# Kernel tuning notes

Measured on AMD Instinct MI355X. Metric: run time of the kernel, lower is better.

The kernel has to match this reference:

```python
import jax, jax.numpy as jnp
import numpy as np

N = 50000
E = 800000
IN = 128
H = 128
OUT = 64
L = 2
THETA = 1.0
SCALE = 2.0


def setup_inputs() -> dict:
    key = jax.random.key(0)
    ks = jax.random.split(key, 12)
    g = lambda k, s: (jax.random.normal(k, s, jnp.float32) * 0.05)
    return {
        "x": jax.random.normal(ks[0], (N, IN), jnp.float32),
        "edge_index": jax.random.randint(ks[1], (2, E), 0, N),
        "mlp_w1": g(ks[2], (IN, 512)), "mlp_b1": jnp.zeros((512,), jnp.float32),
        "mlp_w2": g(ks[3], (512, 64)), "mlp_b2": jnp.zeros((64,), jnp.float32),
        "mlp_w3": g(ks[4], (64, OUT)), "mlp_b3": jnp.zeros((OUT,), jnp.float32),
        "parsing": jnp.ones((L, OUT, OUT), jnp.float32) / SCALE,
        "lin0_w": g(ks[5], (IN, H)), "lin0_b": jnp.zeros((H,), jnp.float32),
        "lin1_w": g(ks[6], (H, OUT)), "lin1_b": jnp.zeros((OUT,), jnp.float32),
        "conv_w1": g(ks[7], (L, H, H)),
        "conv_w2": g(ks[8], (L, H, H)),
    }


def reference(x, edge_index, mlp_w1, mlp_b1, mlp_w2, mlp_b2, mlp_w3, mlp_b3,
              parsing, lin0_w, lin0_b, lin1_w, lin1_b, conv_w1, conv_w2):
    row, col = edge_index[0], edge_index[1]  # start, end

    # --- learn_soft_edge3 (algebraically exact reduction of outer-product + bmm + diag) ---
    h = jax.nn.relu(x @ mlp_w1 + mlp_b1)
    h = jax.nn.relu(h @ mlp_w2 + mlp_b2)
    logits = h @ mlp_w3 + mlp_b3                      # [N, OUT]
    P = jax.nn.relu(SCALE * parsing[0])               # [OUT, OUT]
    # diag(outer(start,end) @ P)[e,c] = start[e,c] * (end @ P)[e,c]
    ew = jnp.sum(logits[row] * (logits @ P)[col], axis=1)  # [E]
    mean = ew.mean()
    var = jnp.var(ew, ddof=1)                          # torch.var is unbiased
    ew = (ew - mean) * jnp.sqrt(jnp.float32(1e-4) / var) + 1.0

    # --- GCN2 stack ---
    x0 = jax.nn.relu(x @ lin0_w + lin0_b)              # [N, H]
    # gcn_norm with self loops (weight 1)
    loop = jnp.arange(N)
    r = jnp.concatenate([row, loop])
    c = jnp.concatenate([col, loop])
    w = jnp.concatenate([ew, jnp.ones((N,), ew.dtype)])
    deg = jax.ops.segment_sum(w, c, num_segments=N)
    dinv = jnp.where(deg > 0, jax.lax.rsqrt(jnp.where(deg > 0, deg, 1.0)), 0.0)
    norm = dinv[r] * w * dinv[c]                       # [E+N]

    hcur = x0
    alpha = 0.0
    for ln in range(L):
        agg = jax.ops.segment_sum(norm[:, None] * hcur[r], c, num_segments=N)  # [N, H]
        agg = agg * (1.0 - alpha)
        x0a = alpha * x0
        beta = float(np.log(THETA / (ln + 1) + 1.0))
        out = (1.0 - beta) * agg + beta * (agg @ conv_w1[ln]) \
            + (1.0 - beta) * x0a + beta * (x0a @ conv_w2[ln])
        hcur = jax.nn.relu(out)
    return hcur @ lin1_w + lin1_b                      # [N, OUT]
```

## Files before the change

### kernel.cpp

```cpp
#include <hip/hip_runtime.h>
#include <hip/hip_bf16.h>
#include <hip/hip_fp16.h>
#include <math.h>

#define NN 50000
#define NE 800000

typedef __attribute__((ext_vector_type(8))) short bf16x8;
typedef __attribute__((ext_vector_type(4))) float f32x4;

__device__ __forceinline__ short f2bf(float f){
  unsigned u = __float_as_uint(f);
  unsigned r = (u + 0x7fffu + ((u >> 16) & 1u)) >> 16;
  return (short)r;
}
__device__ __forceinline__ float bf2f(short s){
  return __uint_as_float(((unsigned)(unsigned short)s) << 16);
}

__device__ __forceinline__ unsigned f2fp8(float f){
  __half h = __float2half(f * 0.00390625f);
  unsigned hb = (unsigned)__half_as_ushort(h);
  unsigned s = hb >> 15;
  unsigned mag = hb & 0x7fffu;
  mag = mag + 0x3fu + ((mag >> 7) & 1u);
  unsigned m8 = mag >> 7;
  if (m8 > 0x7eu) m8 = 0x7eu;
  return (s << 7) | m8;
}
__device__ __forceinline__ void fp8x4_dec(unsigned u, float2& lo, float2& hi){
  unsigned l = ((u & 0x80u) << 8) | ((u & 0x7fu) << 7)
             | ((u & 0x8000u) << 16) | ((u & 0x7f00u) << 15);
  unsigned h = ((u & 0x800000u) >> 8) | ((u & 0x7f0000u) >> 9)
             | (u & 0x80000000u) | ((u & 0x7f000000u) >> 1);
  __half2 hl = *(__half2*)&l;
  __half2 hh = *(__half2*)&h;
  lo = __half22float2(hl);
  hi = __half22float2(hh);
}
__device__ __forceinline__ float fp8_dot4(unsigned a, unsigned b){
  float2 al, ah, bl, bh;
  fp8x4_dec(a, al, ah); fp8x4_dec(b, bl, bh);
  return al.x*bl.x + al.y*bl.y + ah.x*bh.x + ah.y*bh.y;
}

__global__ __launch_bounds__(256) void prep_k(const float* __restrict__ w1,
    const float* __restrict__ w2, const float* __restrict__ w3, const float* __restrict__ pars,
    const float* __restrict__ b3, const float* __restrict__ lin0w, const float* __restrict__ cw1,
    const float* __restrict__ lin1w,
    short* __restrict__ w1t, short* __restrict__ w2t, short* __restrict__ w3t,
    short* __restrict__ w3pt, float* __restrict__ b3P,
    short* __restrict__ lin0wt, short* __restrict__ cw1t0, short* __restrict__ cw1t1,
    short* __restrict__ lin1wt, int* __restrict__ cnt, float* __restrict__ scal){
  int idx = blockIdx.x*256 + threadIdx.x;
  if (idx < NN) cnt[idx] = 0;
  if (idx < 16) scal[idx] = 0.0f;
  if (idx < 65536){
    int n = idx >> 7, k = idx & 127;
    w1t[idx] = f2bf(w1[k*512 + n]);
  } else if (idx < 98304){
    int i = idx - 65536; int n = i >> 9, k = i & 511;
    w2t[i] = f2bf(w2[k*64 + n]);
  } else if (idx < 102400){
    int i = idx - 98304; int n = i >> 6, k = i & 63;
    w3t[i] = f2bf(w3[k*64 + n]);
  } else if (idx < 106496){
    int i = idx - 102400; int c = i >> 6, k = i & 63;
    float s = 0.f;
    for (int j = 0; j < 64; j++)
      s += w3[k*64 + j] * fmaxf(2.f*pars[j*64 + c], 0.f);
    w3pt[i] = f2bf(s);
  } else if (idx < 122880){
    int i = idx - 106496; int n = i >> 7, k = i & 127;
    lin0wt[i] = f2bf(lin0w[k*128 + n]);
  } else if (idx < 139264){
    int i = idx - 122880; int n = i >> 7, k = i & 127;
    cw1t0[i] = f2bf(cw1[k*128 + n]);
  } else if (idx < 155648){
    int i = idx - 139264; int n = i >> 7, k = i & 127;
    cw1t1[i] = f2bf(cw1[16384 + k*128 + n]);
  } else if (idx < 163840){
    int i = idx - 155648; int n = i >> 7, k = i & 127;
    lin1wt[i] = f2bf(lin1w[k*64 + n]);
  } else if (idx < 163904){
    int c = idx - 163840;
    float s = 0.f;
    for (int j = 0; j < 64; j++) s += b3[j] * fmaxf(2.f*pars[j*64 + c], 0.f);
    b3P[c] = s;
  }
}

__global__ __launch_bounds__(256) void mlp_mfma_k(
    const float* __restrict__ x,
    const short* __restrict__ w1t, const float* __restrict__ b1,
    const short* __restrict__ w2t, const float* __restrict__ b2,
    const short* __restrict__ w3t, const float* __restrict__ b3,
    const short* __restrict__ w3pt, const float* __restrict__ b3P,
    unsigned char* __restrict__ lg8, unsigned char* __restrict__ lgp8,
    short* __restrict__ xb, int M)
{
  __shared__ short xs [64][132];
  __shared__ short h1s[64][260];
  __shared__ short h2s[64][68];
  __shared__ short lgs[64][68];
  const int t = threadIdx.x;
  const int wave = t >> 6, lane = t & 63;
  const int quad = lane >> 4, l16 = lane & 15;
  const int m0 = blockIdx.x * 64;

  for (int task = t; task < 1024; task += 256){
    int row = task >> 4, c0 = (task & 15) * 8;
    float4 v0 = make_float4(0,0,0,0), v1 = v0;
    int gm = m0 + row;
    if (gm < M){
      v0 = *(const float4*)(x + (size_t)gm*128 + c0);
      v1 = *(const float4*)(x + (size_t)gm*128 + c0 + 4);
    }
    bf16x8 s;
    s[0]=f2bf(v0.x); s[1]=f2bf(v0.y); s[2]=f2bf(v0.z); s[3]=f2bf(v0.w);
    s[4]=f2bf(v1.x); s[5]=f2bf(v1.y); s[6]=f2bf(v1.z); s[7]=f2bf(v1.w);
    *(bf16x8*)&xs[row][c0] = s;
    if (gm < M) *(bf16x8*)(xb + (size_t)gm*128 + c0) = s;
  }
  __syncthreads();

  f32x4 acc2a[4], acc2b[4];
  #pragma unroll
  for (int mt=0;mt<4;mt++){ acc2a[mt] = (f32x4){0.f,0.f,0.f,0.f}; acc2b[mt] = acc2a[mt]; }
  const int n2 = wave*16 + l16;

  #pragma unroll
  for (int half = 0; half < 2; half++){
    {
      f32x4 acc[4][4];
      #pragma unroll
      for (int mt=0;mt<4;mt++)
        #pragma unroll
        for (int nt=0;nt<4;nt++) acc[mt][nt] = (f32x4){0.f,0.f,0.f,0.f};
      #pragma unroll
      for (int k0 = 0; k0 < 128; k0 += 32){
        bf16x8 a0 = *(const bf16x8*)&xs[l16     ][k0 + quad*8];
        bf16x8 a1 = *(const bf16x8*)&xs[16 + l16][k0 + quad*8];
        bf16x8 a2 = *(const bf16x8*)&xs[32 + l16][k0 + quad*8];
        bf16x8 a3 = *(const bf16x8*)&xs[48 + l16][k0 + quad*8];
        #pragma unroll
        for (int nt = 0; nt < 4; nt++){
          int n = half*256 + wave*64 + nt*16 + l16;
          bf16x8 b = *(const bf16x8*)(w1t + (size_t)n*128 + k0 + quad*8);
          acc[0][nt] = __builtin_amdgcn_mfma_f32_16x16x32_bf16(a0, b, acc[0][nt], 0,0,0);
          acc[1][nt] = __builtin_amdgcn_mfma_f32_16x16x32_bf16(a1, b, acc[1][nt], 0,0,0);
          acc[2][nt] = __builtin_amdgcn_mfma_f32_16x16x32_bf16(a2, b, acc[2][nt], 0,0,0);
          acc[3][nt] = __builtin_amdgcn_mfma_f32_16x16x32_bf16(a3, b, acc[3][nt], 0,0,0);
        }
      }
      #pragma unroll
      for (int nt = 0; nt < 4; nt++){
        int n  = half*256 + wave*64 + nt*16 + l16;
        int cl = wave*64 + nt*16 + l16;
        float bb = b1[n];
        #pragma unroll
        for (int mt = 0; mt < 4; mt++){
          #pragma unroll
          for (int r = 0; r < 4; r++){
            int row = mt*16 + quad*4 + r;
            h1s[row][cl] = f2bf(fmaxf(acc[mt][nt][r] + bb, 0.f));
          }
        }
      }
    }
    __syncthreads();

    #pragma unroll
    for (int k0 = 0; k0 < 128; k0 += 32){
      bf16x8 bA = *(const bf16x8*)(w2t + (size_t)n2*512 + half*256 + k0 + quad*8);
      bf16x8 bB = *(const bf16x8*)(w2t + (size_t)n2*512 + half*256 + 128 + k0 + quad*8);
      #pragma unroll
      for (int mt = 0; mt < 4; mt++){
        bf16x8 aA = *(const bf16x8*)&h1s[mt*16 + l16][k0 + quad*8];
        bf16x8 aB = *(const bf16x8*)&h1s[mt*16 + l16][128 + k0 + quad*8];
        acc2a[mt] = __builtin_amdgcn_mfma_f32_16x16x32_bf16(aA, bA, acc2a[mt], 0,0,0);
        acc2b[mt] = __builtin_amdgcn_mfma_f32_16x16x32_bf16(aB, bB, acc2b[mt], 0,0,0);
      }
    }
    if (half == 0) __syncthreads();
  }

  {
    float bb = b2[n2];
    #pragma unroll
    for (int mt = 0; mt < 4; mt++)
      #pragma unroll
      for (int r = 0; r < 4; r++)
        h2s[mt*16 + quad*4 + r][n2] = f2bf(fmaxf(acc2a[mt][r] + acc2b[mt][r] + bb, 0.f));
  }
  __syncthreads();

  {
    f32x4 accL[4], accP[4];
    #pragma unroll
    for (int mt=0;mt<4;mt++){ accL[mt] = (f32x4){0.f,0.f,0.f,0.f}; accP[mt] = accL[mt]; }
    #pragma unroll
    for (int k0 = 0; k0 < 64; k0 += 32){
      bf16x8 bL = *(const bf16x8*)(w3t  + (size_t)n2*64 + k0 + quad*8);
      bf16x8 bP = *(const bf16x8*)(w3pt + (size_t)n2*64 + k0 + quad*8);
      #pragma unroll
      for (int mt = 0; mt < 4; mt++){
        bf16x8 a = *(const bf16x8*)&h2s[mt*16 + l16][k0 + quad*8];
        accL[mt] = __builtin_amdgcn_mfma_f32_16x16x32_bf16(a, bL, accL[mt], 0,0,0);
        accP[mt] = __builtin_amdgcn_mfma_f32_16x16x32_bf16(a, bP, accP[mt], 0,0,0);
      }
    }
    __syncthreads();
    float bbL = b3[n2], bbP = b3P[n2];
    #pragma unroll
    for (int mt = 0; mt < 4; mt++)
      #pragma unroll
      for (int r = 0; r < 4; r++){
        lgs[mt*16 + quad*4 + r][n2] = f2bf(accL[mt][r] + bbL);
        h2s[mt*16 + quad*4 + r][n2] = f2bf(accP[mt][r] + bbP);
      }
  }
  __syncthreads();

  {
    int row = t >> 2, c0 = (t & 3) * 16;
    int gm = m0 + row;
    if (gm < M){
      const short* pl = &lgs[row][c0];
      const short* pp = &h2s[row][c0];
      unsigned a[4] = {0,0,0,0}, b[4] = {0,0,0,0};
      #pragma unroll
      for (int q2 = 0; q2 < 4; q2++){
        #pragma unroll
        for (int j = 0; j < 4; j++){
          a[q2] |= f2fp8(bf2f(pl[q2*4+j])) << (8*j);
          b[q2] |= f2fp8(bf2f(pp[q2*4+j])) << (8*j);
        }
      }
      uint4 av; av.x=a[0]; av.y=a[1]; av.z=a[2]; av.w=a[3];
      uint4 bv; bv.x=b[0]; bv.y=b[1]; bv.z=b[2]; bv.w=b[3];
      *(uint4*)(lg8  + (size_t)gm*64 + c0) = av;
      *(uint4*)(lgp8 + (size_t)gm*64 + c0) = bv;
    }
  }
}

template<int NT, bool RELU, bool RESID, bool BF16OUT, bool SCALEROW>
__global__ __launch_bounds__(256) void bgemm_k(
    const short* __restrict__ A, const short* __restrict__ Bt,
    const float* __restrict__ bias, const short* __restrict__ extra,
    const float* __restrict__ dinvp,
    float* __restrict__ C, short* __restrict__ Cb, int M, float beta)
{
  const int N = NT*64;
  __shared__ short As[32][132];
  const int t = threadIdx.x;
  const int wave = t >> 6, lane = t & 63;
  const int quad = lane >> 4, l16 = lane & 15;
  const int m0 = blockIdx.x * 32;

  for (int task = t; task < 512; task += 256){
    int row = task >> 4, c0 = (task & 15) * 8;
    bf16x8 v = {0,0,0,0,0,0,0,0};
    if (m0 + row < M) v = *(const bf16x8*)(A + (size_t)(m0+row)*128 + c0);
    *(bf16x8*)&As[row][c0] = v;
  }
  __syncthreads();

  f32x4 acc[2][NT];
  #pragma unroll
  for (int mt=0;mt<2;mt++)
    #pragma unroll
    for (int nt=0;nt<NT;nt++) acc[mt][nt] = (f32x4){0.f,0.f,0.f,0.f};

  #pragma unroll
  for (int k0 = 0; k0 < 128; k0 += 32){
    bf16x8 a0 = *(const bf16x8*)&As[l16     ][k0 + quad*8];
    bf16x8 a1 = *(const bf16x8*)&As[16 + l16][k0 + quad*8];
    #pragma unroll
    for (int nt = 0; nt < NT; nt++){
      int n = (wave*NT + nt)*16 + l16;
      bf16x8 b = *(const bf16x8*)(Bt + (size_t)n*128 + k0 + quad*8);
      acc[0][nt] = __builtin_amdgcn_mfma_f32_16x16x32_bf16(a0, b, acc[0][nt], 0,0,0);
      acc[1][nt] = __builtin_amdgcn_mfma_f32_16x16x32_bf16(a1, b, acc[1][nt], 0,0,0);
    }
  }

  #pragma unroll
  for (int nt = 0; nt < NT; nt++){
    int n = (wave*NT + nt)*16 + l16;
    float bb = (bias != nullptr) ? bias[n] : 0.f;
    #pragma unroll
    for (int mt = 0; mt < 2; mt++){
      #pragma unroll
      for (int r = 0; r < 4; r++){
        int gm = m0 + mt*16 + quad*4 + r;
        if (gm >= M) continue;
        float v = acc[mt][nt][r];
        if (RESID){
          float ex = bf2f(extra[(size_t)gm*N + n]);
          v = beta*v + (1.f - beta)*ex;
        }
        v += bb;
        if (RELU) v = fmaxf(v, 0.f);
        if (SCALEROW) v *= dinvp[gm];
        if (BF16OUT) Cb[(size_t)gm*N + n] = f2bf(v);
        else         C [(size_t)gm*N + n] = v;
      }
    }
  }
}

__global__ __launch_bounds__(256) void bgemm_fuse_k(
    const short* __restrict__ A, const short* __restrict__ Bt,
    const short* __restrict__ extra,
    const short* __restrict__ lin1wt, const float* __restrict__ lin1b,
    float* __restrict__ out, int M, float beta)
{
  __shared__ short As[32][132];
  const int t = threadIdx.x;
  const int wave = t >> 6, lane = t & 63;
  const int quad = lane >> 4, l16 = lane & 15;
  const int m0 = blockIdx.x * 32;

  for (int task = t; task < 512; task += 256){
    int row = task >> 4, c0 = (task & 15) * 8;
    bf16x8 v = {0,0,0,0,0,0,0,0};
    if (m0 + row < M) v = *(const bf16x8*)(A + (size_t)(m0+row)*128 + c0);
    *(bf16x8*)&As[row][c0] = v;
  }
  __syncthreads();

  f32x4 acc[2][2];
  #pragma unroll
  for (int mt=0;mt<2;mt++)
    #pragma unroll
    for (int nt=0;nt<2;nt++) acc[mt][nt] = (f32x4){0.f,0.f,0.f,0.f};

  #pragma unroll
  for (int k0 = 0; k0 < 128; k0 += 32){
    bf16x8 a0 = *(const bf16x8*)&As[l16     ][k0 + quad*8];
    bf16x8 a1 = *(const bf16x8*)&As[16 + l16][k0 + quad*8];
    #pragma unroll
    for (int nt = 0; nt < 2; nt++){
      int n = (wave*2 + nt)*16 + l16;
      bf16x8 b = *(const bf16x8*)(Bt + (size_t)n*128 + k0 + quad*8);
      acc[0][nt] = __builtin_amdgcn_mfma_f32_16x16x32_bf16(a0, b, acc[0][nt], 0,0,0);
      acc[1][nt] = __builtin_amdgcn_mfma_f32_16x16x32_bf16(a1, b, acc[1][nt], 0,0,0);
    }
  }
  __syncthreads();

  #pragma unroll
  for (int nt = 0; nt < 2; nt++){
    int n = (wave*2 + nt)*16 + l16;
    #pragma unroll
    for (int mt = 0; mt < 2; mt++){
      #pragma unroll
      for (int r = 0; r < 4; r++){
        int row = mt*16 + quad*4 + r;
        int gm = m0 + row;
        float v = 0.f;
        if (gm < M){
          float ex = bf2f(extra[(size_t)gm*128 + n]);
          v = fmaxf(beta*acc[mt][nt][r] + (1.f - beta)*ex, 0.f);
        }
        As[row][n] = f2bf(v);
      }
    }
  }
  __syncthreads();

  f32x4 acc2[2];
  acc2[0] = (f32x4){0.f,0.f,0.f,0.f}; acc2[1] = acc2[0];
  const int n2 = wave*16 + l16;
  #pragma unroll
  for (int k0 = 0; k0 < 128; k0 += 32){
    bf16x8 b  = *(const bf16x8*)(lin1wt + (size_t)n2*128 + k0 + quad*8);
    bf16x8 a0 = *(const bf16x8*)&As[l16     ][k0 + quad*8];
    bf16x8 a1 = *(const bf16x8*)&As[16 + l16][k0 + quad*8];
    acc2[0] = __builtin_amdgcn_mfma_f32_16x16x32_bf16(a0, b, acc2[0], 0,0,0);
    acc2[1] = __builtin_amdgcn_mfma_f32_16x16x32_bf16(a1, b, acc2[1], 0,0,0);
  }
  float bb = lin1b[n2];
  #pragma unroll
  for (int mt = 0; mt < 2; mt++)
    #pragma unroll
    for (int r = 0; r < 4; r++){
      int gm = m0 + mt*16 + quad*4 + r;
      if (gm < M) out[(size_t)gm*64 + n2] = acc2[mt][r] + bb;
    }
}

__global__ __launch_bounds__(256) void count_k(const int* __restrict__ col, int* __restrict__ cnt,
    int* __restrict__ rank, int E){
  int i = (blockIdx.x*256 + threadIdx.x)*4;
  if (i + 3 < E){
    int4 c = *(const int4*)(col + i);
    int r0 = atomicAdd(&cnt[c.x], 1);
    int r1 = atomicAdd(&cnt[c.y], 1);
    int r2 = atomicAdd(&cnt[c.z], 1);
    int r3 = atomicAdd(&cnt[c.w], 1);
    *(int4*)(rank + i) = make_int4(r0, r1, r2, r3);
  } else {
    for (; i < E; i++) rank[i] = atomicAdd(&cnt[col[i]], 1);
  }
}

__global__ __launch_bounds__(256) void scan_sums_k(const int* __restrict__ cnt, int* __restrict__ bsum, int n){
  __shared__ int s[256];
  const int t = threadIdx.x;
  int i = blockIdx.x*1024 + t*4;
  int4 v = make_int4(0,0,0,0);
  if (i + 3 < n) v = *(const int4*)(cnt + i);
  else {
    if (i   < n) v.x = cnt[i];
    if (i+1 < n) v.y = cnt[i+1];
    if (i+2 < n) v.z = cnt[i+2];
    if (i+3 < n) v.w = cnt[i+3];
  }
  s[t] = v.x + v.y + v.z + v.w;
  __syncthreads();
  for (int st = 128; st; st >>= 1){
    if (t < st) s[t] += s[t + st];
    __syncthreads();
  }
  if (t == 0) bsum[blockIdx.x] = s[0];
}

__global__ __launch_bounds__(256) void scan_final_k(const int* __restrict__ cnt, const int* __restrict__ bsum,
    int* __restrict__ off, int n, int total, int nb){
  __shared__ int s[256];
  __shared__ int basebs;
  const int t = threadIdx.x;
  if (t < 64){
    int v = (t < nb && t < (int)blockIdx.x) ? bsum[t] : 0;
    #pragma unroll
    for (int o = 1; o < 64; o <<= 1) v += __shfl_xor(v, o);
    if (t == 0) basebs = v;
  }
  int i = blockIdx.x*1024 + t*4;
  int4 v = make_int4(0,0,0,0);
  if (i + 3 < n) v = *(const int4*)(cnt + i);
  else {
    if (i   < n) v.x = cnt[i];
    if (i+1 < n) v.y = cnt[i+1];
    if (i+2 < n) v.z = cnt[i+2];
    if (i+3 < n) v.w = cnt[i+3];
  }
  int tsum = v.x + v.y + v.z + v.w;
  s[t] = tsum;
  __syncthreads();
  #pragma unroll
  for (int st = 1; st < 256; st <<= 1){
    int a = (t >= st) ? s[t - st] : 0;
    __syncthreads();
    s[t] += a;
    __syncthreads();
  }
  int base = s[t] - tsum + basebs;
  int o0 = base, o1 = o0 + v.x, o2 = o1 + v.y, o3 = o2 + v.z;
  if (i   < n) off[i]   = o0;
  if (i+1 < n) off[i+1] = o1;
  if (i+2 < n) off[i+2] = o2;
  if (i+3 < n) off[i+3] = o3;
  if (blockIdx.x == 0 && t == 0) off[n] = total;
}

__global__ __launch_bounds__(256) void scatter_k(const int* __restrict__ row, const int* __restrict__ col,
    const int* __restrict__ off, const int* __restrict__ rank,
    int2* __restrict__ csr_sd, int E){
  int i = (blockIdx.x*256 + threadIdx.x)*4;
  if (i + 3 < E){
    int4 r = *(const int4*)(row + i);
    int4 c = *(const int4*)(col + i);
    int4 k = *(const int4*)(rank + i);
    int o0 = off[c.x], o1 = off[c.y], o2 = off[c.z], o3 = off[c.w];
    int2 p0; p0.x = r.x; p0.y = c.x;
    int2 p1; p1.x = r.y; p1.y = c.y;
    int2 p2; p2.x = r.z; p2.y = c.z;
    int2 p3; p3.x = r.w; p3.y = c.w;
    csr_sd[o0 + k.x] = p0;
    csr_sd[o1 + k.y] = p1;
    csr_sd[o2 + k.z] = p2;
    csr_sd[o3 + k.w] = p3;
  } else {
    for (; i < E; i++){
      int2 p; p.x = row[i]; p.y = col[i];
      csr_sd[off[col[i]] + rank[i]] = p;
    }
  }
}

__global__ __launch_bounds__(256) void ew2_k(const unsigned char* __restrict__ lg8,
    const unsigned char* __restrict__ lgp8,
    const int2* __restrict__ sd,
    float* __restrict__ w, float* __restrict__ scal, int E){
  const int t = threadIdx.x;
  const int lane = t & 63, wid = t >> 6;
  const int g = lane >> 4, q = lane & 15;
  const int gid = (blockIdx.x*4 + wid)*4 + g;
  const int ngroups = gridDim.x*16;
  float s = 0.f, ss = 0.f;
  for (int base = gid*8; base < E; base += ngroups*8){
    int4 p01 = *(const int4*)(sd + base);
    int4 p23 = *(const int4*)(sd + base + 2);
    int4 p45 = *(const int4*)(sd + base + 4);
    int4 p67 = *(const int4*)(sd + base + 6);
    unsigned a0 = *(const unsigned*)(lg8  + (size_t)p01.x*64 + q*4);
    unsigned a1 = *(const unsigned*)(lg8  + (size_t)p01.z*64 + q*4);
    unsigned a2 = *(const unsigned*)(lg8  + (size_t)p23.x*64 + q*4);
    unsigned a3 = *(const unsigned*)(lg8  + (size_t)p23.z*64 + q*4);
    unsigned a4 = *(const unsigned*)(lg8  + (size_t)p45.x*64 + q*4);
    unsigned a5 = *(const unsigned*)(lg8  + (size_t)p45.z*64 + q*4);
    unsigned a6 = *(const unsigned*)(lg8  + (size_t)p67.x*64 + q*4);
    unsigned a7 = *(const unsigned*)(lg8  + (size_t)p67.z*64 + q*4);
    unsigned b0 = *(const unsigned*)(lgp8 + (size_t)p01.y*64 + q*4);
    unsigned b1 = *(const unsigned*)(lgp8 + (size_t)p01.w*64 + q*4);
    unsigned b2 = *(const unsigned*)(lgp8 + (size_t)p23.y*64 + q*4);
    unsigned b3 = *(const unsigned*)(lgp8 + (size_t)p23.w*64 + q*4);
    unsigned b4 = *(const unsigned*)(lgp8 + (size_t)p45.y*64 + q*4);
    unsigned b5 = *(const unsigned*)(lgp8 + (size_t)p45.w*64 + q*4);
    unsigned b6 = *(const unsigned*)(lgp8 + (size_t)p67.y*64 + q*4);
    unsigned b7 = *(const unsigned*)(lgp8 + (size_t)p67.w*64 + q*4);
    float v0 = fp8_dot4(a0, b0);
    float v1 = fp8_dot4(a1, b1);
    float v2 = fp8_dot4(a2, b2);
    float v3 = fp8_dot4(a3, b3);
    float v4 = fp8_dot4(a4, b4);
    float v5 = fp8_dot4(a5, b5);
    float v6 = fp8_dot4(a6, b6);
    float v7 = fp8_dot4(a7, b7);
    #pragma unroll
    for (int o = 1; o < 16; o <<= 1){
      v0 += __shfl_xor(v0, o); v1 += __shfl_xor(v1, o);
      v2 += __shfl_xor(v2, o); v3 += __shfl_xor(v3, o);
      v4 += __shfl_xor(v4, o); v5 += __shfl_xor(v5, o);
      v6 += __shfl_xor(v6, o); v7 += __shfl_xor(v7, o);
    }
    if (q == 0){
      float4 va = make_float4(v0*65536.f, v1*65536.f, v2*65536.f, v3*65536.f);
      float4 vb = make_float4(v4*65536.f, v5*65536.f, v6*65536.f, v7*65536.f);
      *(float4*)(w + base)     = va;
      *(float4*)(w + base + 4) = vb;
      s  += va.x + va.y + va.z + va.w + vb.x + vb.y + vb.z + vb.w;
      ss += va.x*va.x + va.y*va.y + va.z*va.z + va.w*va.w
          + vb.x*vb.x + vb.y*vb.y + vb.z*vb.z + vb.w*vb.w;
    }
  }
  #pragma unroll
  for (int o = 1; o < 64; o <<= 1){ s += __shfl_xor(s, o); ss += __shfl_xor(ss, o); }
  __shared__ float ls[4], lss[4];
  if (lane == 0){ ls[wid] = s; lss[wid] = ss; }
  __syncthreads();
  if (t == 0){
    atomicAdd(&scal[0], ls[0]+ls[1]+ls[2]+ls[3]);
    atomicAdd(&scal[1], lss[0]+lss[1]+lss[2]+lss[3]);
  }
}

__global__ __launch_bounds__(256) void degnorm_k(float* __restrict__ w, const int* __restrict__ off,
    const float* __restrict__ scal, float* __restrict__ dinv, int Nn, int E){
  int n = blockIdx.x*256 + threadIdx.x;
  if (n < Nn){
    double sum = (double)scal[0], sumsq = (double)scal[1];
    double mean_d = sum / (double)E;
    double var    = (sumsq - sum*sum/(double)E) / (double)(E-1);
    float mean = (float)mean_d;
    float k    = (float)sqrt(1e-4 / var);
    int s = off[n], e = off[n+1];
    float d = 1.0f;
    for (int j = s; j < e; j++){
      float v = (w[j] - mean) * k + 1.0f;
      w[j] = v;
      d += v;
    }
    dinv[n] = (d > 0.f) ? rsqrtf(d) : 0.f;
  }
}

__global__ __launch_bounds__(256) void agg_gather_k(const short* __restrict__ hb,
    const int* __restrict__ off, const int2* __restrict__ sd, const float* __restrict__ w,
    const float* __restrict__ dinv, short* __restrict__ aggb, int Nn){
  int n = blockIdx.x*4 + (threadIdx.x >> 6);
  int lane = threadIdx.x & 63;
  if (n >= Nn) return;
  float d = dinv[n];
  short2 hv = *(const short2*)(hb + (size_t)n*128 + lane*2);
  float acc0 = bf2f(hv.x), acc1 = bf2f(hv.y);
  int s = off[n], e = off[n+1];
  int j = s;
  for (; j + 7 < e; j += 8){
    int4 p0 = *(const int4*)(sd + j);
    int4 p1 = *(const int4*)(sd + j + 2);
    int4 p2 = *(const int4*)(sd + j + 4);
    int4 p3 = *(const int4*)(sd + j + 6);
    float4 w0 = *(const float4*)(w + j);
    float4 w1 = *(const float4*)(w + j + 4);
    short2 h0 = *(const short2*)(hb + (size_t)p0.x*128 + lane*2);
    short2 h1 = *(const short2*)(hb + (size_t)p0.z*128 + lane*2);
    short2 h2 = *(const short2*)(hb + (size_t)p1.x*128 + lane*2);
    short2 h3 = *(const short2*)(hb + (size_t)p1.z*128 + lane*2);
    short2 h4 = *(const short2*)(hb + (size_t)p2.x*128 + lane*2);
    short2 h5 = *(const short2*)(hb + (size_t)p2.z*128 + lane*2);
    short2 h6 = *(const short2*)(hb + (size_t)p3.x*128 + lane*2);
    short2 h7 = *(const short2*)(hb + (size_t)p3.z*128 + lane*2);
    acc0 += w0.x*bf2f(h0.x) + w0.y*bf2f(h1.x) + w0.z*bf2f(h2.x) + w0.w*bf2f(h3.x)
          + w1.x*bf2f(h4.x) + w1.y*bf2f(h5.x) + w1.z*bf2f(h6.x) + w1.w*bf2f(h7.x);
    acc1 += w0.x*bf2f(h0.y) + w0.y*bf2f(h1.y) + w0.z*bf2f(h2.y) + w0.w*bf2f(h3.y)
          + w1.x*bf2f(h4.y) + w1.y*bf2f(h5.y) + w1.z*bf2f(h6.y) + w1.w*bf2f(h7.y);
  }
  for (; j < e; j++){
    int2 p = sd[j];
    short2 h0 = *(const short2*)(hb + (size_t)p.x*128 + lane*2);
    float w0 = w[j];
    acc0 += w0*bf2f(h0.x); acc1 += w0*bf2f(h0.y);
  }
  acc0 *= d; acc1 *= d;
  short2 o; o.x = f2bf(acc0); o.y = f2bf(acc1);
  *(short2*)(aggb + (size_t)n*128 + lane*2) = o;
}

extern "C" void kernel_launch(void* const* d_in, const int* in_sizes, int n_in,
                              void* d_out, int out_size, void* d_ws, size_t ws_size,
                              hipStream_t stream){
  const float* x      = (const float*)d_in[0];
  const int*   ei     = (const int*)  d_in[1];
  const float* w1     = (const float*)d_in[2];
  const float* b1     = (const float*)d_in[3];
  const float* w2     = (const float*)d_in[4];
  const float* b2     = (const float*)d_in[5];
  const float* w3     = (const float*)d_in[6];
  const float* b3     = (const float*)d_in[7];
  const float* pars   = (const float*)d_in[8];
  const float* lin0w  = (const float*)d_in[9];
  const float* lin0b  = (const float*)d_in[10];
  const float* lin1w  = (const float*)d_in[11];
  const float* lin1b  = (const float*)d_in[12];
  const float* cw1    = (const float*)d_in[13];
  float* out          = (float*)d_out;

  float* ws = (float*)d_ws;
  int*   cnt     = (int*)(ws + 0);
  int*   off     = (int*)(ws + 50048);
  int2*  csr_sd  = (int2*)(ws + 150144);
  int*   bsum    = (int*)(ws + 1750400);
  short* lin0wt  = (short*)(ws + 1751000);
  short* cw1t0   = lin0wt + 16384;
  short* cw1t1   = cw1t0 + 16384;
  short* lin1wt  = cw1t1 + 16384;
  unsigned char* lg8  = (unsigned char*)(ws + 1800000);
  unsigned char* lgp8 = (unsigned char*)(ws + 2600000);
  float* csr_w2  = ws + 3400000;
  float* dinv    = ws + 5800000;
  float* scal    = ws + 5850048;
  float* b3P     = ws + 5850064;
  short* bufAb   = (short*)(ws + 5900000);
  short* bufCb   = (short*)(ws + 9100000);
  short* aggb    = (short*)(ws + 12300000);
  short* w1t     = (short*)(ws + 18700000);
  short* w2t     = w1t + 65536;
  short* w3t     = w2t + 32768;
  short* w3pt    = w3t + 4096;
  short* xb      = (short*)(ws + 18800000);
  int*   rank    = (int*)(ws + 22000000);

  const int Mn = NN, E = NE;
  const int* erow = ei;
  const int* ecol = ei + E;
  const float beta0 = 0.69314718055994530942f;
  const float beta1 = 0.40546510810816438198f;
  const int nScanB = (Mn + 1023) / 1024;
  const int nGB = (Mn + 31) / 32;
  const int nE4 = (E/4 + 255) / 256;

  prep_k<<<(163904+255)/256, 256, 0, stream>>>(w1, w2, w3, pars, b3, lin0w, cw1, lin1w,
                                               w1t, w2t, w3t, w3pt, b3P,
                                               lin0wt, cw1t0, cw1t1, lin1wt, cnt, scal);
  count_k<<<nE4, 256, 0, stream>>>(ecol, cnt, rank, E);
  scan_sums_k<<<nScanB, 256, 0, stream>>>(cnt, bsum, Mn);
  scan_final_k<<<nScanB, 256, 0, stream>>>(cnt, bsum, off, Mn, E, nScanB);
  scatter_k<<<nE4, 256, 0, stream>>>(erow, ecol, off, rank, csr_sd, E);
  mlp_mfma_k<<<(Mn+63)/64, 256, 0, stream>>>(x, w1t, b1, w2t, b2, w3t, b3, w3pt, b3P,
                                             lg8, lgp8, xb, Mn);
  ew2_k<<<1024, 256, 0, stream>>>(lg8, lgp8, csr_sd, csr_w2, scal, E);
  degnorm_k<<<(Mn+255)/256, 256, 0, stream>>>(csr_w2, off, scal, dinv, Mn, E);
  bgemm_k<2,true,false,true,true><<<nGB, 256, 0, stream>>>(xb, lin0wt, lin0b, nullptr, dinv, nullptr, bufAb, Mn, 0.f);
  agg_gather_k<<<(Mn+3)/4, 256, 0, stream>>>(bufAb, off, csr_sd, csr_w2, dinv, aggb, Mn);
  bgemm_k<2,true,true,true,true><<<nGB, 256, 0, stream>>>(aggb, cw1t0, nullptr, aggb, dinv, nullptr, bufCb, Mn, beta0);
  agg_gather_k<<<(Mn+3)/4, 256, 0, stream>>>(bufCb, off, csr_sd, csr_w2, dinv, aggb, Mn);
  bgemm_fuse_k<<<nGB, 256, 0, stream>>>(aggb, cw1t1, aggb, lin1wt, lin1b, out, Mn, beta1);
}
```

Before: 360.8 us.

## Fuse neighbor aggregation gather into the following conv GEMM kernels

Replaces the separate agg_gather_k plus GEMM launches with a templated agg_bgemm_k that gathers the 32 aggregated rows of a block directly into shared memory and then runs the MFMA conv GEMM on them, with the last layer also applying lin1. This removes the aggregated-feature round trip through global memory and two kernel launches. In exchange, each block's 4 waves each gather 8 rows serially before the MFMA stage, which reduces gather parallelism and latency hiding compared with one wave per node across many blocks.

```diff
diff --git a/kernel.cpp b/kernel.cpp
--- a/kernel.cpp
+++ b/kernel.cpp
@@ -311,11 +311,14 @@
   }
 }
 
-__global__ __launch_bounds__(256) void bgemm_fuse_k(
-    const short* __restrict__ A, const short* __restrict__ Bt,
-    const short* __restrict__ extra,
+template<bool LAST>
+__global__ __launch_bounds__(256) void agg_bgemm_k(
+    const short* __restrict__ hb,
+    const int* __restrict__ off, const int2* __restrict__ sd, const float* __restrict__ w,
+    const float* __restrict__ dinv,
+    const short* __restrict__ Bt,
     const short* __restrict__ lin1wt, const float* __restrict__ lin1b,
-    float* __restrict__ out, int M, float beta)
+    short* __restrict__ Cb, float* __restrict__ out, int M, float beta)
 {
   __shared__ short As[32][132];
   const int t = threadIdx.x;
@@ -323,11 +326,46 @@
   const int quad = lane >> 4, l16 = lane & 15;
   const int m0 = blockIdx.x * 32;
 
-  for (int task = t; task < 512; task += 256){
-    int row = task >> 4, c0 = (task & 15) * 8;
-    bf16x8 v = {0,0,0,0,0,0,0,0};
-    if (m0 + row < M) v = *(const bf16x8*)(A + (size_t)(m0+row)*128 + c0);
-    *(bf16x8*)&As[row][c0] = v;
+  for (int rr = 0; rr < 8; rr++){
+    int row = wave*8 + rr;
+    int n = m0 + row;
+    float acc0 = 0.f, acc1 = 0.f;
+    if (n < M){
+      float d = dinv[n];
+      short2 hv = *(const short2*)(hb + (size_t)n*128 + lane*2);
+      acc0 = bf2f(hv.x); acc1 = bf2f(hv.y);
+      int s = off[n], e = off[n+1];
+      int j = s;
+      for (; j + 7 < e; j += 8){
+        int4 p0 = *(const int4*)(sd + j);
+        int4 p1 = *(const int4*)(sd + j + 2);
+        int4 p2 = *(const int4*)(sd + j + 4);
+        int4 p3 = *(const int4*)(sd + j + 6);
+        float4 w0 = *(const float4*)(w + j);
+        float4 w1 = *(const float4*)(w + j + 4);
+        short2 h0 = *(const short2*)(hb + (size_t)p0.x*128 + lane*2);
+        short2 h1 = *(const short2*)(hb + (size_t)p0.z*128 + lane*2);
+        short2 h2 = *(const short2*)(hb + (size_t)p1.x*128 + lane*2);
+        short2 h3 = *(const short2*)(hb + (size_t)p1.z*128 + lane*2);
+        short2 h4 = *(const short2*)(hb + (size_t)p2.x*128 + lane*2);
+        short2 h5 = *(const short2*)(hb + (size_t)p2.z*128 + lane*2);
+        short2 h6 = *(const short2*)(hb + (size_t)p3.x*128 + lane*2);
+        short2 h7 = *(const short2*)(hb + (size_t)p3.z*128 + lane*2);
+        acc0 += w0.x*bf2f(h0.x) + w0.y*bf2f(h1.x) + w0.z*bf2f(h2.x) + w0.w*bf2f(h3.x)
+              + w1.x*bf2f(h4.x) + w1.y*bf2f(h5.x) + w1.z*bf2f(h6.x) + w1.w*bf2f(h7.x);
+        acc1 += w0.x*bf2f(h0.y) + w0.y*bf2f(h1.y) + w0.z*bf2f(h2.y) + w0.w*bf2f(h3.y)
+              + w1.x*bf2f(h4.y) + w1.y*bf2f(h5.y) + w1.z*bf2f(h6.y) + w1.w*bf2f(h7.y);
+      }
+      for (; j < e; j++){
+        int2 p = sd[j];
+        short2 h0 = *(const short2*)(hb + (size_t)p.x*128 + lane*2);
+        float w0 = w[j];
+        acc0 += w0*bf2f(h0.x); acc1 += w0*bf2f(h0.y);
+      }
+      acc0 *= d; acc1 *= d;
+    }
+    short2 o; o.x = f2bf(acc0); o.y = f2bf(acc1);
+    *(short2*)&As[row][lane*2] = o;
   }
   __syncthreads();
 
@@ -336,7 +374,6 @@
   for (int mt=0;mt<2;mt++)
     #pragma unroll
     for (int nt=0;nt<2;nt++) acc[mt][nt] = (f32x4){0.f,0.f,0.f,0.f};
-
   #pragma unroll
   for (int k0 = 0; k0 < 128; k0 += 32){
     bf16x8 a0 = *(const bf16x8*)&As[l16     ][k0 + quad*8];
@@ -349,47 +386,70 @@
       acc[1][nt] = __builtin_amdgcn_mfma_f32_16x16x32_bf16(a1, b, acc[1][nt], 0,0,0);
     }
   }
-  __syncthreads();
-
-  #pragma unroll
-  for (int nt = 0; nt < 2; nt++){
-    int n = (wave*2 + nt)*16 + l16;
-    #pragma unroll
-    for (int mt = 0; mt < 2; mt++){
+
+  if (!LAST){
+    #pragma unroll
+    for (int nt = 0; nt < 2; nt++){
+      int n = (wave*2 + nt)*16 + l16;
+      #pragma unroll
+      for (int mt = 0; mt < 2; mt++){
+        #pragma unroll
+        for (int r = 0; r < 4; r++){
+          int row = mt*16 + quad*4 + r;
+          int gm = m0 + row;
+          if (gm >= M) continue;
+          float ex = bf2f(As[row][n]);
+          float v = fmaxf(beta*acc[mt][nt][r] + (1.f - beta)*ex, 0.f) * dinv[gm];
+          Cb[(size_t)gm*128 + n] = f2bf(v);
+        }
+      }
+    }
+  } else {
+    short hloc[2][2][4];
+    #pragma unroll
+    for (int nt = 0; nt < 2; nt++){
+      int n = (wave*2 + nt)*16 + l16;
+      #pragma unroll
+      for (int mt = 0; mt < 2; mt++)
+        #pragma unroll
+        for (int r = 0; r < 4; r++){
+          int row = mt*16 + quad*4 + r;
+          float ex = bf2f(As[row][n]);
+          hloc[nt][mt][r] = f2bf(fmaxf(beta*acc[mt][nt][r] + (1.f - beta)*ex, 0.f));
+        }
+    }
+    __syncthreads();
+    #pragma unroll
+    for (int nt = 0; nt < 2; nt++){
+      int n = (wave*2 + nt)*16 + l16;
+      #pragma unroll
+      for (int mt = 0; mt < 2; mt++)
+        #pragma unroll
+        for (int r = 0; r < 4; r++)
+          As[mt*16 + quad*4 + r][n] = hloc[nt][mt][r];
+    }
+    __syncthreads();
+
+    f32x4 acc2[2];
+    acc2[0] = (f32x4){0.f,0.f,0.f,0.f}; acc2[1] = acc2[0];
+    const int n2 = wave*16 + l16;
+    #pragma unroll
+    for (int k0 = 0; k0 < 128; k0 += 32){
+      bf16x8 b  = *(const bf16x8*)(lin1wt + (size_t)n2*128 + k0 + quad*8);
+      bf16x8 a0 = *(const bf16x8*)&As[l16     ][k0 + quad*8];
+      bf16x8 a1 = *(const bf16x8*)&As[16 + l16][k0 + quad*8];
+      acc2[0] = __builtin_amdgcn_mfma_f32_16x16x32_bf16(a0, b, acc2[0], 0,0,0);
+      acc2[1] = __builtin_amdgcn_mfma_f32_16x16x32_bf16(a1, b, acc2[1], 0,0,0);
+    }
+    float bb = lin1b[n2];
+    #pragma unroll
+    for (int mt = 0; mt < 2; mt++)
       #pragma unroll
       for (int r = 0; r < 4; r++){
-        int row = mt*16 + quad*4 + r;
-        int gm = m0 + row;
-        float v = 0.f;
-        if (gm < M){
-          float ex = bf2f(extra[(size_t)gm*128 + n]);
-          v = fmaxf(beta*acc[mt][nt][r] + (1.f - beta)*ex, 0.f);
-        }
-        As[row][n] = f2bf(v);
-      }
-    }
-  }
-  __syncthreads();
-
-  f32x4 acc2[2];
-  acc2[0] = (f32x4){0.f,0.f,0.f,0.f}; acc2[1] = acc2[0];
-  const int n2 = wave*16 + l16;
-  #pragma unroll
-  for (int k0 = 0; k0 < 128; k0 += 32){
-    bf16x8 b  = *(const bf16x8*)(lin1wt + (size_t)n2*128 + k0 + quad*8);
-    bf16x8 a0 = *(const bf16x8*)&As[l16     ][k0 + quad*8];
-    bf16x8 a1 = *(const bf16x8*)&As[16 + l16][k0 + quad*8];
-    acc2[0] = __builtin_amdgcn_mfma_f32_16x16x32_bf16(a0, b, acc2[0], 0,0,0);
-    acc2[1] = __builtin_amdgcn_mfma_f32_16x16x32_bf16(a1, b, acc2[1], 0,0,0);
-  }
-  float bb = lin1b[n2];
-  #pragma unroll
-  for (int mt = 0; mt < 2; mt++)
-    #pragma unroll
-    for (int r = 0; r < 4; r++){
-      int gm = m0 + mt*16 + quad*4 + r;
-      if (gm < M) out[(size_t)gm*64 + n2] = acc2[mt][r] + bb;
-    }
+        int gm = m0 + mt*16 + quad*4 + r;
+        if (gm < M) out[(size_t)gm*64 + n2] = acc2[mt][r] + bb;
+      }
+  }
 }
 
 __global__ __launch_bounds__(256) void count_k(const int* __restrict__ col, int* __restrict__ cnt,
@@ -579,48 +639,6 @@
   }
 }
 
-__global__ __launch_bounds__(256) void agg_gather_k(const short* __restrict__ hb,
-    const int* __restrict__ off, const int2* __restrict__ sd, const float* __restrict__ w,
-    const float* __restrict__ dinv, short* __restrict__ aggb, int Nn){
-  int n = blockIdx.x*4 + (threadIdx.x >> 6);
-  int lane = threadIdx.x & 63;
-  if (n >= Nn) return;
-  float d = dinv[n];
-  short2 hv = *(const short2*)(hb + (size_t)n*128 + lane*2);
-  float acc0 = bf2f(hv.x), acc1 = bf2f(hv.y);
-  int s = off[n], e = off[n+1];
-  int j = s;
-  for (; j + 7 < e; j += 8){
-    int4 p0 = *(const int4*)(sd + j);
-    int4 p1 = *(const int4*)(sd + j + 2);
-    int4 p2 = *(const int4*)(sd + j + 4);
-    int4 p3 = *(const int4*)(sd + j + 6);
-    float4 w0 = *(const float4*)(w + j);
-    float4 w1 = *(const float4*)(w + j + 4);
-    short2 h0 = *(const short2*)(hb + (size_t)p0.x*128 + lane*2);
-    short2 h1 = *(const short2*)(hb + (size_t)p0.z*128 + lane*2);
-    short2 h2 = *(const short2*)(hb + (size_t)p1.x*128 + lane*2);
-    short2 h3 = *(const short2*)(hb + (size_t)p1.z*128 + lane*2);
-    short2 h4 = *(const short2*)(hb + (size_t)p2.x*128 + lane*2);
-    short2 h5 = *(const short2*)(hb + (size_t)p2.z*128 + lane*2);
-    short2 h6 = *(const short2*)(hb + (size_t)p3.x*128 + lane*2);
-    short2 h7 = *(const short2*)(hb + (size_t)p3.z*128 + lane*2);
-    acc0 += w0.x*bf2f(h0.x) + w0.y*bf2f(h1.x) + w0.z*bf2f(h2.x) + w0.w*bf2f(h3.x)
-          + w1.x*bf2f(h4.x) + w1.y*bf2f(h5.x) + w1.z*bf2f(h6.x) + w1.w*bf2f(h7.x);
-    acc1 += w0.x*bf2f(h0.y) + w0.y*bf2f(h1.y) + w0.z*bf2f(h2.y) + w0.w*bf2f(h3.y)
-          + w1.x*bf2f(h4.y) + w1.y*bf2f(h5.y) + w1.z*bf2f(h6.y) + w1.w*bf2f(h7.y);
-  }
-  for (; j < e; j++){
-    int2 p = sd[j];
-    short2 h0 = *(const short2*)(hb + (size_t)p.x*128 + lane*2);
-    float w0 = w[j];
-    acc0 += w0*bf2f(h0.x); acc1 += w0*bf2f(h0.y);
-  }
-  acc0 *= d; acc1 *= d;
-  short2 o; o.x = f2bf(acc0); o.y = f2bf(acc1);
-  *(short2*)(aggb + (size_t)n*128 + lane*2) = o;
-}
-
 extern "C" void kernel_launch(void* const* d_in, const int* in_sizes, int n_in,
                               void* d_out, int out_size, void* d_ws, size_t ws_size,
                               hipStream_t stream){
@@ -657,7 +675,6 @@
   float* b3P     = ws + 5850064;
   short* bufAb   = (short*)(ws + 5900000);
   short* bufCb   = (short*)(ws + 9100000);
-  short* aggb    = (short*)(ws + 12300000);
   short* w1t     = (short*)(ws + 18700000);
   short* w2t     = w1t + 65536;
   short* w3t     = w2t + 32768;
@@ -686,8 +703,8 @@
   ew2_k<<<1024, 256, 0, stream>>>(lg8, lgp8, csr_sd, csr_w2, scal, E);
   degnorm_k<<<(Mn+255)/256, 256, 0, stream>>>(csr_w2, off, scal, dinv, Mn, E);
   bgemm_k<2,true,false,true,true><<<nGB, 256, 0, stream>>>(xb, lin0wt, lin0b, nullptr, dinv, nullptr, bufAb, Mn, 0.f);
-  agg_gather_k<<<(Mn+3)/4, 256, 0, stream>>>(bufAb, off, csr_sd, csr_w2, dinv, aggb, Mn);
-  bgemm_k<2,true,true,true,true><<<nGB, 256, 0, stream>>>(aggb, cw1t0, nullptr, aggb, dinv, nullptr, bufCb, Mn, beta0);
-  agg_gather_k<<<(Mn+3)/4, 256, 0, stream>>>(bufCb, off, csr_sd, csr_w2, dinv, aggb, Mn);
-  bgemm_fuse_k<<<nGB, 256, 0, stream>>>(aggb, cw1t1, aggb, lin1wt, lin1b, out, Mn, beta1);
-}
+  agg_bgemm_k<false><<<nGB, 256, 0, stream>>>(bufAb, off, csr_sd, csr_w2, dinv,
+                                              cw1t0, nullptr, nullptr, bufCb, nullptr, Mn, beta0);
+  agg_bgemm_k<true><<<nGB, 256, 0, stream>>>(bufCb, off, csr_sd, csr_w2, dinv,
+                                             cw1t1, lin1wt, lin1b, nullptr, out, Mn, beta1);
+}
```

New measurement: 381.5 us. 1.06x slower.
